# Kernel optimization log

Hardware: AMD Instinct MI355X
Metric: run time of the kernel (lower is better)

## Reference

```python
import jax, jax.numpy as jnp
import numpy as np

B, N, D = 4, 4096, 1024
HEADS, DIM_HEAD = 16, 64
INNER = HEADS * DIM_HEAD
LN_EPS = 1e-5


def next_fast_len(n):
    # smallest 5-smooth integer >= n (matches scipy.fftpack.next_fast_len)
    while True:
        m = n
        for p in (2, 3, 5):
            while m % p == 0:
                m //= p
        if m == 1:
            return n
        n += 1


def setup_inputs() -> dict:
    key = jax.random.key(0)
    k = jax.random.split(key, 6)
    x = jax.random.normal(k[0], (B, N, D), dtype=jnp.float32)
    gamma = jnp.ones((D,), dtype=jnp.float32)
    beta = jnp.zeros((D,), dtype=jnp.float32)
    alpha = jax.random.normal(k[1], (HEADS,), dtype=jnp.float32)
    w_in = jax.random.normal(k[2], (INNER, D), dtype=jnp.float32) * 0.02
    w_out = jax.random.normal(k[3], (D, INNER), dtype=jnp.float32) * 0.02
    return {"x": x, "gamma": gamma, "beta": beta, "alpha": alpha, "w_in": w_in, "w_out": w_out}


def reference(x, gamma, beta, alpha, w_in, w_out):
    b, n, d = x.shape
    h, dh = HEADS, DIM_HEAD
    # LayerNorm (biased variance, eps=1e-5)
    mu = jnp.mean(x, axis=-1, keepdims=True)
    var = jnp.var(x, axis=-1, keepdims=True)
    xn = (x - mu) * jax.lax.rsqrt(var + LN_EPS) * gamma + beta
    # project_in (no bias), split heads: b n (h d) -> b h n d
    xi = jnp.einsum('bnd,ed->bne', xn, w_in)
    xi = xi.reshape(b, n, h, dh).transpose(0, 2, 1, 3)  # [b,h,n,dh]
    # exponential decay weights per head: alpha * (1-alpha)**flip(arange(n)) -> [h, n]
    a = jax.nn.sigmoid(alpha)[:, None]
    weights = a * (1.0 - a) ** jnp.arange(n - 1, -1, -1, dtype=x.dtype)[None, :]
    # FFT-based causal correlation (conv1d_fft)
    fast_len = next_fast_len(n + n - 1)
    f_x = jnp.fft.rfft(xi, n=fast_len, axis=-2)           # [b,h,L',dh] complex
    f_w = jnp.fft.rfft(weights, n=fast_len, axis=-1)      # [h,L'] complex
    out = jnp.fft.irfft(f_x * jnp.conj(f_w)[None, :, :, None], fast_len, axis=-2)
    out = jnp.roll(out, -1, axis=-2)
    out = out[:, :, fast_len - n:, :]                      # last n positions -> [b,h,n,dh]
    # merge heads and project out
    out = out.transpose(0, 2, 1, 3).reshape(b, n, h * dh)
    return jnp.einsum('bne,de->bnd', out, w_out)
```

## Files before the change

### kernel.cpp

```cpp
#include <hip/hip_runtime.h>
#include <hip/hip_bf16.h>

#define B_ 4
#define N_ 4096
#define D_ 1024
#define H_ 16
#define INNER_ 1024
#define M_ (B_ * N_)
#define CH_ 128
#define CL_ 32

using bf16x8 = __attribute__((ext_vector_type(8))) __bf16;
using f32x4  = __attribute__((ext_vector_type(4))) float;

__device__ __forceinline__ float bf2f(unsigned short v) {
  return __uint_as_float(((unsigned)v) << 16);
}
__device__ __forceinline__ unsigned short f2bf(float f) {
  __hip_bfloat16 h = __float2bfloat16(f);
  return *reinterpret_cast<unsigned short*>(&h);
}
__device__ __forceinline__ float sigm(float x) { return 1.f / (1.f + expf(-x)); }

__device__ __forceinline__ void gload_lds16(const void* g, void* l) {
  __builtin_amdgcn_global_load_lds(
      (const __attribute__((address_space(1))) unsigned int*)g,
      (__attribute__((address_space(3))) unsigned int*)l, 16, 0, 0);
}

#define W4_ ((INNER_ * D_) / 4)
__global__ __launch_bounds__(256) void cast2_kernel(
    const float* __restrict__ wa, const float* __restrict__ wb,
    __hip_bfloat16* __restrict__ oa, __hip_bfloat16* __restrict__ ob) {
  int i = blockIdx.x * 256 + threadIdx.x;
  const float* src = (i < W4_) ? wa : wb;
  __hip_bfloat16* dst = (i < W4_) ? oa : ob;
  int j = (i < W4_) ? i : i - W4_;
  float4 v = reinterpret_cast<const float4*>(src)[j];
  ushort4 o;
  o.x = f2bf(v.x); o.y = f2bf(v.y); o.z = f2bf(v.z); o.w = f2bf(v.w);
  reinterpret_cast<ushort4*>(dst)[j] = o;
}

__global__ __launch_bounds__(256) void ln_kernel(
    const float* __restrict__ x, const float* __restrict__ gamma,
    const float* __restrict__ beta, __hip_bfloat16* __restrict__ xn) {
  const long row = blockIdx.x;
  const int t = threadIdx.x;
  const float4 v = reinterpret_cast<const float4*>(x + row * D_)[t];
  float s = v.x + v.y + v.z + v.w;
  float s2 = v.x * v.x + v.y * v.y + v.z * v.z + v.w * v.w;
#pragma unroll
  for (int o = 32; o > 0; o >>= 1) {
    s += __shfl_down(s, o);
    s2 += __shfl_down(s2, o);
  }
  __shared__ float red[8];
  const int lane = t & 63, wv = t >> 6;
  if (lane == 0) { red[wv] = s; red[4 + wv] = s2; }
  __syncthreads();
  const float sum = red[0] + red[1] + red[2] + red[3];
  const float sum2 = red[4] + red[5] + red[6] + red[7];
  const float mu = sum * (1.f / D_);
  const float var = sum2 * (1.f / D_) - mu * mu;
  const float rs = rsqrtf(var + 1e-5f);
  const float4 g = reinterpret_cast<const float4*>(gamma)[t];
  const float4 bb = reinterpret_cast<const float4*>(beta)[t];
  ushort4 o;
  o.x = f2bf((v.x - mu) * rs * g.x + bb.x);
  o.y = f2bf((v.y - mu) * rs * g.y + bb.y);
  o.z = f2bf((v.z - mu) * rs * g.z + bb.z);
  o.w = f2bf((v.w - mu) * rs * g.w + bb.w);
  reinterpret_cast<ushort4*>(xn + row * D_)[t] = o;
}

__device__ __forceinline__ void stc(float* p, float v) { *p = v; }
__device__ __forceinline__ void stc(__hip_bfloat16* p, float v) { *p = __float2bfloat16(v); }

template <typename TOUT, int NT>
__global__ __launch_bounds__(512, 2) void gemm256_kernel(
    const __hip_bfloat16* __restrict__ A, const __hip_bfloat16* __restrict__ Bt,
    TOUT* __restrict__ C, int M, int N, int K) {
  static_assert(NT >= 4, "ring needs >=4 tiles");
  __shared__ __align__(16) char lds[131072];
  const int tid = threadIdx.x;
  const int lane = tid & 63;
  const int wave = tid >> 6;

  int wg = blockIdx.y * gridDim.x + blockIdx.x;
  wg = (wg & 7) * 32 + (wg >> 3);
  const int bx = wg & 3;
  const int by = wg >> 2;
  const long bm = (long)by * 256;
  const long bn = (long)bx * 256;

  const int u0  = (tid & 7) ^ ((tid >> 3) & 7);
  const int r0  = 2 * (tid >> 3) + (u0 >> 2);
  const int ck0 = u0 & 3;
  const __hip_bfloat16* sA0 = A  + (bm + r0) * (long)K + ck0 * 8;
  const __hip_bfloat16* sA1 = sA0 + 128l * K;
  const __hip_bfloat16* sB0 = Bt + (bn + r0) * (long)K + ck0 * 8;
  const __hip_bfloat16* sB1 = sB0 + 128l * K;
  char* dbase = (char*)lds + wave * 1024;

  const int wm = wave >> 2;
  const int wn = wave & 3;
  const int fr = lane & 15;
  const int ck = lane >> 4;
  const int pos = (((fr & 1) << 2) | ck) ^ ((fr >> 1) & 7);
  const int laneA = wm * 8192 + (fr >> 1) * 128 + pos * 16;
  const int laneB = 16384 + wn * 4096 + (fr >> 1) * 128 + pos * 16;

  f32x4 acc[8][4] = {};

#define STAGE_A(kt) do { const int _s = (kt) & 3;                         \
    gload_lds16(sA0 + (long)(kt) * 32, dbase + _s * 32768);               \
    gload_lds16(sA1 + (long)(kt) * 32, dbase + _s * 32768 + 8192); } while (0)
#define STAGE_B(kt) do { const int _s = (kt) & 3;                         \
    gload_lds16(sB0 + (long)(kt) * 32, dbase + _s * 32768 + 16384);       \
    gload_lds16(sB1 + (long)(kt) * 32, dbase + _s * 32768 + 24576); } while (0)
#define SBAR() asm volatile("s_barrier" ::: "memory")
#define SCHED0() __builtin_amdgcn_sched_barrier(0)

  STAGE_A(0); STAGE_B(0);
  STAGE_A(1); STAGE_B(1);
  asm volatile("s_waitcnt vmcnt(4)" ::: "memory");
  SBAR();

#pragma unroll 4
  for (int t = 0; t < NT; ++t) {
    const char* base = (const char*)lds + (t & 3) * 32768;
    bf16x8 bv[4], av[4], av2[4];
#pragma unroll
    for (int c = 0; c < 4; ++c) bv[c] = *(const bf16x8*)(base + laneB + c * 1024);
#pragma unroll
    for (int r = 0; r < 4; ++r) av[r] = *(const bf16x8*)(base + laneA + r * 1024);
    if (t + 2 < NT) STAGE_A(t + 2);
    SCHED0();
    SBAR();
    asm volatile("s_waitcnt lgkmcnt(0)" ::: "memory");
    SCHED0();
    __builtin_amdgcn_s_setprio(1);
#pragma unroll
    for (int r = 0; r < 4; ++r)
#pragma unroll
      for (int c = 0; c < 4; ++c)
        acc[r][c] = __builtin_amdgcn_mfma_f32_16x16x32_bf16(av[r], bv[c], acc[r][c], 0, 0, 0);
    __builtin_amdgcn_s_setprio(0);
    SCHED0();
    SBAR();
#pragma unroll
    for (int r = 0; r < 4; ++r) av2[r] = *(const bf16x8*)(base + laneA + (r + 4) * 1024);
    if (t + 2 < NT) STAGE_B(t + 2);
    SCHED0();
    SBAR();
    asm volatile("s_waitcnt lgkmcnt(0)" ::: "memory");
    SCHED0();
    __builtin_amdgcn_s_setprio(1);
#pragma unroll
    for (int r = 0; r < 4; ++r)
#pragma unroll
      for (int c = 0; c < 4; ++c)
        acc[r + 4][c] = __builtin_amdgcn_mfma_f32_16x16x32_bf16(av2[r], bv[c], acc[r + 4][c], 0, 0, 0);
    __builtin_amdgcn_s_setprio(0);
    SCHED0();
    if (t < NT - 2)       asm volatile("s_waitcnt vmcnt(4)" ::: "memory");
    else if (t == NT - 2) asm volatile("s_waitcnt vmcnt(0)" ::: "memory");
    SBAR();
  }
#undef STAGE_A
#undef STAGE_B
#undef SBAR
#undef SCHED0

  const int cr = ck * 4;
#pragma unroll
  for (int rf = 0; rf < 8; ++rf)
#pragma unroll
    for (int cf = 0; cf < 4; ++cf)
#pragma unroll
      for (int r = 0; r < 4; ++r) {
        const long row = bm + wm * 128 + rf * 16 + cr + r;
        const long col = bn + wn * 64 + cf * 16 + fr;
        stc(&C[row * (long)N + col], acc[rf][cf][r]);
      }
}

__global__ __launch_bounds__(256) void scan_finals_kernel(
    const __hip_bfloat16* __restrict__ xi, float* __restrict__ finals,
    const float* __restrict__ alpha) {
  const int e0 = threadIdx.x * 4;
  const int c = blockIdx.y;
  const int b = blockIdx.z;
  const float a = sigm(alpha[e0 >> 6]);
  const float om = 1.f - a;
  long base = ((long)b * N_ + (long)c * CL_) * INNER_ + e0;
  float y0 = 0.f, y1 = 0.f, y2 = 0.f, y3 = 0.f;
  for (int t = 0; t < CL_; ++t) {
    ushort4 u = *(const ushort4*)(xi + base);
    y0 = om * y0 + a * bf2f(u.x);
    y1 = om * y1 + a * bf2f(u.y);
    y2 = om * y2 + a * bf2f(u.z);
    y3 = om * y3 + a * bf2f(u.w);
    base += INNER_;
  }
  float4 f4 = make_float4(y0, y1, y2, y3);
  *reinterpret_cast<float4*>(&finals[((long)b * CH_ + c) * INNER_ + e0]) = f4;
}

__global__ __launch_bounds__(256) void scan_carry_kernel(
    const float* __restrict__ finals, float* __restrict__ carries,
    const float* __restrict__ alpha) {
  const int g = blockIdx.x * 256 + threadIdx.x;
  const int b = g >> 10;
  const int e = g & 1023;
  const float a = sigm(alpha[e >> 6]);
  const float dc = powf(1.f - a, (float)CL_);
  float carry = 0.f;
  for (int c = 0; c < CH_; ++c) {
    const long idx = ((long)b * CH_ + c) * INNER_ + e;
    carries[idx] = carry;
    carry = finals[idx] + dc * carry;
  }
}

__global__ __launch_bounds__(256) void scan_apply_kernel(
    const __hip_bfloat16* __restrict__ xi, __hip_bfloat16* __restrict__ y,
    const float* __restrict__ carries, const float* __restrict__ alpha) {
  const int e0 = threadIdx.x * 4;
  const int c = blockIdx.y;
  const int b = blockIdx.z;
  const float a = sigm(alpha[e0 >> 6]);
  const float om = 1.f - a;
  const float4 cr = *reinterpret_cast<const float4*>(
      &carries[((long)b * CH_ + c) * INNER_ + e0]);
  float y0 = cr.x, y1 = cr.y, y2 = cr.z, y3 = cr.w;
  long base = ((long)b * N_ + (long)c * CL_) * INNER_ + e0;
  for (int t = 0; t < CL_; ++t) {
    ushort4 u = *(const ushort4*)(xi + base);
    y0 = om * y0 + a * bf2f(u.x);
    y1 = om * y1 + a * bf2f(u.y);
    y2 = om * y2 + a * bf2f(u.z);
    y3 = om * y3 + a * bf2f(u.w);
    ushort4 o;
    o.x = f2bf(y0); o.y = f2bf(y1); o.z = f2bf(y2); o.w = f2bf(y3);
    *(ushort4*)(y + base) = o;
    base += INNER_;
  }
}

extern "C" void kernel_launch(void* const* d_in, const int* in_sizes, int n_in,
                              void* d_out, int out_size, void* d_ws, size_t ws_size,
                              hipStream_t stream) {
  const float* x     = (const float*)d_in[0];
  const float* gamma = (const float*)d_in[1];
  const float* beta  = (const float*)d_in[2];
  const float* alpha = (const float*)d_in[3];
  const float* w_in  = (const float*)d_in[4];
  const float* w_out = (const float*)d_in[5];
  float* out = (float*)d_out;
  char* ws = (char*)d_ws;

  __hip_bfloat16* xn = (__hip_bfloat16*)ws;
  __hip_bfloat16* wi = (__hip_bfloat16*)(ws + (32l << 20));
  __hip_bfloat16* wo = (__hip_bfloat16*)(ws + (34l << 20));
  float* finals      = (float*)(ws + (36l << 20));
  float* carries     = (float*)(ws + (38l << 20));
  __hip_bfloat16* xi = (__hip_bfloat16*)d_out;

  cast2_kernel<<<2048, 256, 0, stream>>>(w_in, w_out, wi, wo);

  ln_kernel<<<M_, 256, 0, stream>>>(x, gamma, beta, xn);

  gemm256_kernel<__hip_bfloat16, 32>
      <<<dim3(INNER_ / 256, M_ / 256), 512, 0, stream>>>(xn, wi, xi, M_, INNER_, D_);

  __hip_bfloat16* y = xn;
  scan_finals_kernel<<<dim3(1, CH_, B_), 256, 0, stream>>>(xi, finals, alpha);
  scan_carry_kernel<<<(B_ * INNER_) / 256, 256, 0, stream>>>(finals, carries, alpha);
  scan_apply_kernel<<<dim3(1, CH_, B_), 256, 0, stream>>>(xi, y, carries, alpha);

  gemm256_kernel<float, 32>
      <<<dim3(D_ / 256, M_ / 256), 512, 0, stream>>>(y, wo, out, M_, D_, INNER_);
}
```

Before: 132.9 us.

## Switch GEMM to 32x32x16 MFMA, simplify pipeline, fuse LN with weight cast

The GEMM inner loop now uses 32x32x16 bf16 MFMA tiles instead of 16x16x32, with a new LDS fragment addressing and epilogue mapping. The split half-iteration schedule with extra barriers and priority hints is replaced by one load-then-compute step per k-tile. The loop is fully unrolled and the occupancy hint is dropped. The weight cast and LayerNorm are merged into one launch to save a kernel launch. These changes aim to cut LDS reads and barrier overhead, but they lose the finer overlap of loads and MFMA work and may raise register pressure.

After: 130.4 us. Within noise of the previous version (-1.9%).

```diff
diff --git a/kernel.cpp b/kernel.cpp
--- a/kernel.cpp
+++ b/kernel.cpp
@@ -10,8 +10,9 @@
 #define CH_ 128
 #define CL_ 32
 
-using bf16x8 = __attribute__((ext_vector_type(8))) __bf16;
-using f32x4  = __attribute__((ext_vector_type(4))) float;
+using bf16x8  = __attribute__((ext_vector_type(8))) __bf16;
+using f32x4   = __attribute__((ext_vector_type(4))) float;
+using f32x16  = __attribute__((ext_vector_type(16))) float;
 
 __device__ __forceinline__ float bf2f(unsigned short v) {
   return __uint_as_float(((unsigned)v) << 16);
@@ -29,23 +30,23 @@
 }
 
 #define W4_ ((INNER_ * D_) / 4)
-__global__ __launch_bounds__(256) void cast2_kernel(
+__global__ __launch_bounds__(256) void lncast_kernel(
+    const float* __restrict__ x, const float* __restrict__ gamma,
+    const float* __restrict__ beta, __hip_bfloat16* __restrict__ xn,
     const float* __restrict__ wa, const float* __restrict__ wb,
     __hip_bfloat16* __restrict__ oa, __hip_bfloat16* __restrict__ ob) {
-  int i = blockIdx.x * 256 + threadIdx.x;
-  const float* src = (i < W4_) ? wa : wb;
-  __hip_bfloat16* dst = (i < W4_) ? oa : ob;
-  int j = (i < W4_) ? i : i - W4_;
-  float4 v = reinterpret_cast<const float4*>(src)[j];
-  ushort4 o;
-  o.x = f2bf(v.x); o.y = f2bf(v.y); o.z = f2bf(v.z); o.w = f2bf(v.w);
-  reinterpret_cast<ushort4*>(dst)[j] = o;
-}
-
-__global__ __launch_bounds__(256) void ln_kernel(
-    const float* __restrict__ x, const float* __restrict__ gamma,
-    const float* __restrict__ beta, __hip_bfloat16* __restrict__ xn) {
-  const long row = blockIdx.x;
+  if (blockIdx.x < 2048) {
+    int i = blockIdx.x * 256 + threadIdx.x;
+    const float* src = (i < W4_) ? wa : wb;
+    __hip_bfloat16* dst = (i < W4_) ? oa : ob;
+    int j = (i < W4_) ? i : i - W4_;
+    float4 v = reinterpret_cast<const float4*>(src)[j];
+    ushort4 o;
+    o.x = f2bf(v.x); o.y = f2bf(v.y); o.z = f2bf(v.z); o.w = f2bf(v.w);
+    reinterpret_cast<ushort4*>(dst)[j] = o;
+    return;
+  }
+  const long row = blockIdx.x - 2048;
   const int t = threadIdx.x;
   const float4 v = reinterpret_cast<const float4*>(x + row * D_)[t];
   float s = v.x + v.y + v.z + v.w;
@@ -78,7 +79,7 @@
 __device__ __forceinline__ void stc(__hip_bfloat16* p, float v) { *p = __float2bfloat16(v); }
 
 template <typename TOUT, int NT>
-__global__ __launch_bounds__(512, 2) void gemm256_kernel(
+__global__ __launch_bounds__(512) void gemm256_kernel(
     const __hip_bfloat16* __restrict__ A, const __hip_bfloat16* __restrict__ Bt,
     TOUT* __restrict__ C, int M, int N, int K) {
   static_assert(NT >= 4, "ring needs >=4 tiles");
@@ -97,7 +98,7 @@
   const int u0  = (tid & 7) ^ ((tid >> 3) & 7);
   const int r0  = 2 * (tid >> 3) + (u0 >> 2);
   const int ck0 = u0 & 3;
-  const __hip_bfloat16* sA0 = A  + (bm + r0) * (long)K + ck0 * 8;
+  const __hip_bfloat16* sA0 = A + (bm + r0) * (long)K + ck0 * 8;
   const __hip_bfloat16* sA1 = sA0 + 128l * K;
   const __hip_bfloat16* sB0 = Bt + (bn + r0) * (long)K + ck0 * 8;
   const __hip_bfloat16* sB1 = sB0 + 128l * K;
@@ -105,13 +106,16 @@
 
   const int wm = wave >> 2;
   const int wn = wave & 3;
-  const int fr = lane & 15;
-  const int ck = lane >> 4;
-  const int pos = (((fr & 1) << 2) | ck) ^ ((fr >> 1) & 7);
-  const int laneA = wm * 8192 + (fr >> 1) * 128 + pos * 16;
-  const int laneB = 16384 + wn * 4096 + (fr >> 1) * 128 + pos * 16;
-
-  f32x4 acc[8][4] = {};
+  const int l31 = lane & 31;
+  const int lh  = lane >> 5;
+  const int ub = ((lane & 1) << 2) | lh;
+  const int ux = (l31 >> 1) & 7;
+  const int uk0 = (ub ^ ux) * 16;
+  const int uk1 = ((ub | 2) ^ ux) * 16;
+  const int pA = wm * 8192 + (l31 >> 1) * 128;
+  const int pB = 16384 + wn * 4096 + (l31 >> 1) * 128;
+
+  f32x16 acc[4][2] = {};
 
 #define STAGE_A(kt) do { const int _s = (kt) & 3;                         \
     gload_lds16(sA0 + (long)(kt) * 32, dbase + _s * 32768);               \
@@ -119,70 +123,51 @@
 #define STAGE_B(kt) do { const int _s = (kt) & 3;                         \
     gload_lds16(sB0 + (long)(kt) * 32, dbase + _s * 32768 + 16384);       \
     gload_lds16(sB1 + (long)(kt) * 32, dbase + _s * 32768 + 24576); } while (0)
-#define SBAR() asm volatile("s_barrier" ::: "memory")
-#define SCHED0() __builtin_amdgcn_sched_barrier(0)
 
   STAGE_A(0); STAGE_B(0);
   STAGE_A(1); STAGE_B(1);
   asm volatile("s_waitcnt vmcnt(4)" ::: "memory");
-  SBAR();
-
-#pragma unroll 4
+  asm volatile("s_barrier" ::: "memory");
+
+#pragma unroll
   for (int t = 0; t < NT; ++t) {
     const char* base = (const char*)lds + (t & 3) * 32768;
-    bf16x8 bv[4], av[4], av2[4];
-#pragma unroll
-    for (int c = 0; c < 4; ++c) bv[c] = *(const bf16x8*)(base + laneB + c * 1024);
-#pragma unroll
-    for (int r = 0; r < 4; ++r) av[r] = *(const bf16x8*)(base + laneA + r * 1024);
-    if (t + 2 < NT) STAGE_A(t + 2);
-    SCHED0();
-    SBAR();
-    asm volatile("s_waitcnt lgkmcnt(0)" ::: "memory");
-    SCHED0();
-    __builtin_amdgcn_s_setprio(1);
-#pragma unroll
-    for (int r = 0; r < 4; ++r)
-#pragma unroll
-      for (int c = 0; c < 4; ++c)
-        acc[r][c] = __builtin_amdgcn_mfma_f32_16x16x32_bf16(av[r], bv[c], acc[r][c], 0, 0, 0);
-    __builtin_amdgcn_s_setprio(0);
-    SCHED0();
-    SBAR();
-#pragma unroll
-    for (int r = 0; r < 4; ++r) av2[r] = *(const bf16x8*)(base + laneA + (r + 4) * 1024);
-    if (t + 2 < NT) STAGE_B(t + 2);
-    SCHED0();
-    SBAR();
-    asm volatile("s_waitcnt lgkmcnt(0)" ::: "memory");
-    SCHED0();
-    __builtin_amdgcn_s_setprio(1);
-#pragma unroll
-    for (int r = 0; r < 4; ++r)
-#pragma unroll
-      for (int c = 0; c < 4; ++c)
-        acc[r + 4][c] = __builtin_amdgcn_mfma_f32_16x16x32_bf16(av2[r], bv[c], acc[r + 4][c], 0, 0, 0);
-    __builtin_amdgcn_s_setprio(0);
-    SCHED0();
-    if (t < NT - 2)       asm volatile("s_waitcnt vmcnt(4)" ::: "memory");
-    else if (t == NT - 2) asm volatile("s_waitcnt vmcnt(0)" ::: "memory");
-    SBAR();
+    bf16x8 av[4][2], bv[2][2];
+#pragma unroll
+    for (int cb = 0; cb < 2; ++cb) {
+      bv[cb][0] = *(const bf16x8*)(base + pB + cb * 2048 + uk0);
+      bv[cb][1] = *(const bf16x8*)(base + pB + cb * 2048 + uk1);
+    }
+#pragma unroll
+    for (int rb = 0; rb < 4; ++rb) {
+      av[rb][0] = *(const bf16x8*)(base + pA + rb * 2048 + uk0);
+      av[rb][1] = *(const bf16x8*)(base + pA + rb * 2048 + uk1);
+    }
+    if (t + 2 < NT) { STAGE_A(t + 2); STAGE_B(t + 2); }
+#pragma unroll
+    for (int ks = 0; ks < 2; ++ks)
+#pragma unroll
+      for (int rb = 0; rb < 4; ++rb)
+#pragma unroll
+        for (int cb = 0; cb < 2; ++cb)
+          acc[rb][cb] = __builtin_amdgcn_mfma_f32_32x32x16_bf16(
+              av[rb][ks], bv[cb][ks], acc[rb][cb], 0, 0, 0);
+    if (t + 2 < NT)      asm volatile("s_waitcnt vmcnt(4)" ::: "memory");
+    else if (t + 1 < NT) asm volatile("s_waitcnt vmcnt(0)" ::: "memory");
+    if (t + 1 < NT)      asm volatile("s_barrier" ::: "memory");
   }
 #undef STAGE_A
 #undef STAGE_B
-#undef SBAR
-#undef SCHED0
-
-  const int cr = ck * 4;
-#pragma unroll
-  for (int rf = 0; rf < 8; ++rf)
-#pragma unroll
-    for (int cf = 0; cf < 4; ++cf)
-#pragma unroll
-      for (int r = 0; r < 4; ++r) {
-        const long row = bm + wm * 128 + rf * 16 + cr + r;
-        const long col = bn + wn * 64 + cf * 16 + fr;
-        stc(&C[row * (long)N + col], acc[rf][cf][r]);
+
+#pragma unroll
+  for (int rb = 0; rb < 4; ++rb)
+#pragma unroll
+    for (int cb = 0; cb < 2; ++cb)
+#pragma unroll
+      for (int r = 0; r < 16; ++r) {
+        const long row = bm + wm * 128 + rb * 32 + (r & 3) + 8 * (r >> 2) + 4 * lh;
+        const long col = bn + wn * 64 + cb * 32 + l31;
+        stc(&C[row * (long)N + col], acc[rb][cb][r]);
       }
 }
 
@@ -268,9 +253,7 @@
   float* carries     = (float*)(ws + (38l << 20));
   __hip_bfloat16* xi = (__hip_bfloat16*)d_out;
 
-  cast2_kernel<<<2048, 256, 0, stream>>>(w_in, w_out, wi, wo);
-
-  ln_kernel<<<M_, 256, 0, stream>>>(x, gamma, beta, xn);
+  lncast_kernel<<<2048 + M_, 256, 0, stream>>>(x, gamma, beta, xn, w_in, w_out, wi, wo);
 
   gemm256_kernel<__hip_bfloat16, 32>
       <<<dim3(INNER_ / 256, M_ / 256), 512, 0, stream>>>(xn, wi, xi, M_, INNER_, D_);
```
